# Performance work log

Measured on AMD Instinct MI355X. Metric: run time of the kernel, lower is better.

Reference implementation:

```python
import jax, jax.numpy as jnp
import numpy as np
import math

B, T, D_IN, D_OUT = 4, 2048, 2048, 2048

def _inv_sigmoid(v):
    return math.log(v / (1 - v + 1e-08))

def setup_inputs() -> dict:
    key = jax.random.key(0)
    ks = jax.random.split(key, 6)
    x = jax.random.normal(ks[0], (B, T, D_IN), dtype=jnp.float32)
    W_p = jax.random.normal(ks[1], (D_OUT, D_IN), dtype=jnp.float32) * 0.02
    W_i = jax.random.normal(ks[2], (D_OUT, D_IN), dtype=jnp.float32) * 0.002
    W_d = jax.random.normal(ks[3], (D_OUT, D_IN), dtype=jnp.float32) * 0.002
    alpha_logit = jnp.full((D_IN,), _inv_sigmoid(0.9), dtype=jnp.float32)
    beta_logit = jnp.full((D_IN,), _inv_sigmoid(0.5), dtype=jnp.float32)
    W_gate_w = jax.random.normal(ks[4], (3, 3 * D_IN), dtype=jnp.float32) * 0.01
    W_gate_b = jnp.array([1.0, 0.0, 0.0], dtype=jnp.float32)
    bias = jnp.zeros((D_OUT,), dtype=jnp.float32)
    return {"x": x, "W_p": W_p, "W_i": W_i, "W_d": W_d,
            "alpha_logit": alpha_logit, "beta_logit": beta_logit,
            "W_gate_w": W_gate_w, "W_gate_b": W_gate_b, "bias": bias}

def _pid_features(x, alpha, beta):
    # x: (B,T,D). Single scan computing EMA integral and smoothed derivative.
    x_t = jnp.swapaxes(x, 0, 1)  # (T,B,D)
    x_prev = jnp.concatenate([jnp.zeros_like(x_t[:1]), x_t[:-1]], axis=0)
    diff_t = x_t - x_prev  # raw finite difference
    def step(carry, inp):
        s, d = carry
        xt, dt = inp
        s = alpha * s + (1.0 - alpha) * xt
        d = beta * d + (1.0 - beta) * dt
        return (s, d), (s, d)
    s0 = jnp.zeros(x.shape[::2], dtype=x.dtype)  # (B,D)
    _, (integ_t, deriv_t) = jax.lax.scan(step, (s0, s0), (x_t, diff_t))
    return jnp.swapaxes(integ_t, 0, 1), jnp.swapaxes(deriv_t, 0, 1)

def reference(x, W_p, W_i, W_d, alpha_logit, beta_logit, W_gate_w, W_gate_b, bias):
    alpha = jax.nn.sigmoid(alpha_logit)  # (D,)
    beta = jax.nn.sigmoid(beta_logit)
    integral, derivative = _pid_features(x, alpha, beta)  # (B,T,D) each
    gate_in = jnp.concatenate([x, integral, derivative], axis=-1)  # (B,T,3D)
    logits = jnp.einsum('btk,gk->btg', gate_in, W_gate_w) + W_gate_b
    gates = jax.nn.softmax(logits, axis=-1)  # (B,T,3)
    p_out = jnp.einsum('btd,od->bto', x, W_p)
    i_out = jnp.einsum('btd,od->bto', integral, W_i)
    d_out = jnp.einsum('btd,od->bto', derivative, W_d)
    y = gates[..., 0:1] * p_out + gates[..., 1:2] * i_out + gates[..., 2:3] * d_out + bias
    return y
```

## Files before the change

### kernel.cpp

```cpp
#include <hip/hip_runtime.h>
#include <stdint.h>

typedef unsigned short u16;

#define GAS __attribute__((address_space(1)))
#define LAS __attribute__((address_space(3)))

typedef __bf16 bf16x8 __attribute__((ext_vector_type(8)));
typedef float f32x4 __attribute__((ext_vector_type(4)));


__device__ inline u16 f2b(float f) {
    uint32_t x = __float_as_uint(f);
    uint32_t r = (x + 0x7fffu + ((x >> 16) & 1u)) >> 16;
    return (u16)r;
}

__device__ inline float b2f(u16 u) {
    union { uint32_t i; float f; } v;
    v.i = ((uint32_t)u) << 16;
    return v.f;
}

__device__ inline void load8b(float* v, const u16* p) {
    uint4 u = *(const uint4*)p;
    v[0] = b2f((u16)(u.x)); v[1] = b2f((u16)(u.x >> 16));
    v[2] = b2f((u16)(u.y)); v[3] = b2f((u16)(u.y >> 16));
    v[4] = b2f((u16)(u.z)); v[5] = b2f((u16)(u.z >> 16));
    v[6] = b2f((u16)(u.w)); v[7] = b2f((u16)(u.w >> 16));
}

__device__ inline void load8f(float* v, const float* p) {
    float4 a = *(const float4*)p;
    float4 b = *(const float4*)(p + 4);
    v[0] = a.x; v[1] = a.y; v[2] = a.z; v[3] = a.w;
    v[4] = b.x; v[5] = b.y; v[6] = b.z; v[7] = b.w;
}

__device__ inline void store8b(u16* p, const float* v, float scale) {
    uint4 u;
    u.x = (uint32_t)f2b(v[0] * scale) | ((uint32_t)f2b(v[1] * scale) << 16);
    u.y = (uint32_t)f2b(v[2] * scale) | ((uint32_t)f2b(v[3] * scale) << 16);
    u.z = (uint32_t)f2b(v[4] * scale) | ((uint32_t)f2b(v[5] * scale) << 16);
    u.w = (uint32_t)f2b(v[6] * scale) | ((uint32_t)f2b(v[7] * scale) << 16);
    *(uint4*)p = u;
}

__device__ inline float sigmoidf(float v) { return 1.f / (1.f + __expf(-v)); }

__device__ inline float pow64f(float a) {
    float p = a * a;
    p = p * p;
    p = p * p;
    p = p * p;
    p = p * p;
    return p * p;
}

__device__ inline float* carry_ptr(u16* Z, int plane, int b, int c, int d) {
    int f = ((plane * 4 + b) * 32 + c) * 2048 + d;
    int row = f >> 10;
    int off = f & 1023;
    return (float*)(Z + (size_t)row * 6144) + off;
}

__global__ __launch_bounds__(256) void pack_w(
    const float* __restrict__ Wp, const float* __restrict__ Wi,
    const float* __restrict__ Wd, u16* __restrict__ Wcat)
{
    int i = (blockIdx.x * 256 + threadIdx.x) * 8;
    int seg = i >> 22;
    int j = i & 4194303;
    const float* src = (seg == 0) ? Wp : (seg == 1) ? Wi : Wd;
    int o = j >> 11;
    int c = j & 2047;
    float v[8];
    load8f(v, src + j);
    store8b(Wcat + (size_t)o * 6144 + seg * 2048 + c, v, 1.0f);
}

__global__ __launch_bounds__(256) void scan_pass1(
    const float* __restrict__ x, const float* __restrict__ alog,
    const float* __restrict__ blog, u16* __restrict__ Z)
{
    const int d = (blockIdx.x * 256 + threadIdx.x) * 2;
    const int c = blockIdx.y;
    const int b = blockIdx.z;
    const float2 al2 = *(const float2*)(alog + d);
    const float2 bl2 = *(const float2*)(blog + d);
    const float a0 = sigmoidf(al2.x), a1 = sigmoidf(al2.y);
    const float e0 = sigmoidf(bl2.x), e1 = sigmoidf(bl2.y);
    const float oa0 = 1.f - a0, oa1 = 1.f - a1;
    const float oe0 = 1.f - e0, oe1 = 1.f - e1;
    const float* xp = x + ((size_t)b * 2048 + c * 64) * 2048 + d;
    float px0 = 0.f, px1 = 0.f;
    if (c != 0) { float2 t = *(const float2*)(xp - 2048); px0 = t.x; px1 = t.y; }
    float s0 = 0.f, s1 = 0.f, d0 = 0.f, d1 = 0.f;
    #pragma unroll 8
    for (int t = 0; t < 64; ++t) {
        float2 xf = *(const float2*)(xp + (size_t)t * 2048);
        s0 = a0 * s0 + oa0 * xf.x;
        s1 = a1 * s1 + oa1 * xf.y;
        d0 = e0 * d0 + oe0 * (xf.x - px0);
        d1 = e1 * d1 + oe1 * (xf.y - px1);
        px0 = xf.x; px1 = xf.y;
    }
    *(float2*)carry_ptr(Z, 0, b, c, d) = make_float2(s0, s1);
    *(float2*)carry_ptr(Z, 1, b, c, d) = make_float2(d0, d1);
}

__global__ __launch_bounds__(256) void scan_pass2(
    const float* __restrict__ alog, const float* __restrict__ blog,
    u16* __restrict__ Z)
{
    const int g = blockIdx.x * 256 + threadIdx.x;
    const int b = g >> 11;
    const int d = g & 2047;
    const float aL = pow64f(sigmoidf(alog[d]));
    const float bL = pow64f(sigmoidf(blog[d]));
    float sIn = 0.f, dIn = 0.f;
    for (int c = 0; c < 32; ++c) {
        float* sp = carry_ptr(Z, 0, b, c, d);
        float* dp = carry_ptr(Z, 1, b, c, d);
        float sl = *sp, dl = *dp;
        *sp = sIn; *dp = dIn;
        sIn = sl + aL * sIn;
        dIn = dl + bL * dIn;
    }
}

__global__ __launch_bounds__(256) void scan_pass3(
    const float* __restrict__ x, const float* __restrict__ alog,
    const float* __restrict__ blog, u16* __restrict__ Z)
{
    const int d = (blockIdx.x * 256 + threadIdx.x) * 2;
    const int c = blockIdx.y;
    const int b = blockIdx.z;
    const float2 al2 = *(const float2*)(alog + d);
    const float2 bl2 = *(const float2*)(blog + d);
    const float a0 = sigmoidf(al2.x), a1 = sigmoidf(al2.y);
    const float e0 = sigmoidf(bl2.x), e1 = sigmoidf(bl2.y);
    const float oa0 = 1.f - a0, oa1 = 1.f - a1;
    const float oe0 = 1.f - e0, oe1 = 1.f - e1;
    const float* xp = x + ((size_t)b * 2048 + c * 64) * 2048 + d;
    u16* zp = Z + ((size_t)b * 2048 + c * 64) * 6144 + 2048 + d;
    float2 sc = *(const float2*)carry_ptr(Z, 0, b, c, d);
    float2 dc = *(const float2*)carry_ptr(Z, 1, b, c, d);
    float s0 = sc.x, s1 = sc.y, d0 = dc.x, d1 = dc.y;
    float px0 = 0.f, px1 = 0.f;
    if (c != 0) { float2 t = *(const float2*)(xp - 2048); px0 = t.x; px1 = t.y; }
    #pragma unroll 8
    for (int t = 0; t < 64; ++t) {
        float2 xf = *(const float2*)(xp + (size_t)t * 2048);
        s0 = a0 * s0 + oa0 * xf.x;
        s1 = a1 * s1 + oa1 * xf.y;
        d0 = e0 * d0 + oe0 * (xf.x - px0);
        d1 = e1 * d1 + oe1 * (xf.y - px1);
        px0 = xf.x; px1 = xf.y;
        size_t zo = (size_t)t * 6144;
        *(uint32_t*)(zp + zo) = (uint32_t)f2b(s0) | ((uint32_t)f2b(s1) << 16);
        *(uint32_t*)(zp + zo + 2048) = (uint32_t)f2b(d0) | ((uint32_t)f2b(d1) << 16);
    }
}

__global__ __launch_bounds__(256) void gates_kernel(
    const float* __restrict__ x, const float* __restrict__ Wg,
    const float* __restrict__ Wgb, u16* __restrict__ Z)
{
    const int row = blockIdx.x;
    const int tid = threadIdx.x;
    const int k = tid * 8;
    const float* xr = x + (size_t)row * 2048;
    u16* zr = Z + (size_t)row * 6144;

    float xv[8], sv[8], dv[8];
    load8f(xv, xr + k);
    load8b(sv, zr + 2048 + k);
    load8b(dv, zr + 4096 + k);

    float p[3];
    #pragma unroll
    for (int gg = 0; gg < 3; ++gg) {
        float wx[8], ws[8], wd[8];
        load8f(wx, Wg + gg * 6144 + k);
        load8f(ws, Wg + gg * 6144 + 2048 + k);
        load8f(wd, Wg + gg * 6144 + 4096 + k);
        float acc = 0.f;
        #pragma unroll
        for (int j = 0; j < 8; ++j)
            acc += xv[j] * wx[j] + sv[j] * ws[j] + dv[j] * wd[j];
        p[gg] = acc;
    }

    #pragma unroll
    for (int off = 32; off > 0; off >>= 1) {
        p[0] += __shfl_down(p[0], off);
        p[1] += __shfl_down(p[1], off);
        p[2] += __shfl_down(p[2], off);
    }

    __shared__ float red[4][3];
    __shared__ float gsh[3];
    int wv = tid >> 6, lane = tid & 63;
    if (lane == 0) { red[wv][0] = p[0]; red[wv][1] = p[1]; red[wv][2] = p[2]; }
    __syncthreads();
    if (tid == 0) {
        float l0 = red[0][0] + red[1][0] + red[2][0] + red[3][0] + Wgb[0];
        float l1 = red[0][1] + red[1][1] + red[2][1] + red[3][1] + Wgb[1];
        float l2 = red[0][2] + red[1][2] + red[2][2] + red[3][2] + Wgb[2];
        float m = fmaxf(l0, fmaxf(l1, l2));
        float e0 = __expf(l0 - m), e1 = __expf(l1 - m), e2 = __expf(l2 - m);
        float inv = 1.f / (e0 + e1 + e2);
        gsh[0] = e0 * inv; gsh[1] = e1 * inv; gsh[2] = e2 * inv;
    }
    __syncthreads();
    float g0 = gsh[0], g1 = gsh[1], g2 = gsh[2];
    store8b(zr + k, xv, g0);
    store8b(zr + 2048 + k, sv, g1);
    store8b(zr + 4096 + k, dv, g2);
}

__global__ __launch_bounds__(512, 2) void gemm_kernel(
    const u16* __restrict__ Z, const u16* __restrict__ Wcat,
    const float* __restrict__ bias, float* __restrict__ out)
{
    extern __shared__ u16 lds[];
    u16* const lA = lds;
    u16* const lB = lds + 32768;

    const int tid = threadIdx.x;
    const int bn = blockIdx.x * 256;
    const int bm = blockIdx.y * 256;

    const int sr  = tid >> 3;
    const int scq = (tid & 7) ^ (sr & 7);
    const u16* aglob = Z    + (size_t)(bm + sr) * 6144 + scq * 8;
    const u16* bglob = Wcat + (size_t)(bn + sr) * 6144 + scq * 8;

    const int lane = tid & 63;
    const int wv = tid >> 6;
    const int wm = wv & 1;
    const int wn = wv >> 1;
    const int fr = lane & 15;
    const int fq = lane >> 4;
    const int chlo = fq ^ (fr & 7);
    const int aoff = fr * 64 + chlo * 8;
    const int boff = ((wn & 1) * 64 + fr) * 64 + chlo * 8;
    const int aoffh = aoff ^ 32;
    const int boffh = boff ^ 32;

    f32x4 acc[8][4] = {};

#define GLOAD(gsrc, ldst)                                                     \
    __builtin_amdgcn_global_load_lds((const GAS uint32_t*)(gsrc),             \
                                     (LAS uint32_t*)(ldst), 16, 0, 0)

    GLOAD(bglob,                        lB + tid * 8);
    GLOAD(bglob + (size_t) 64 * 6144,   lB + 4096 + tid * 8);
    GLOAD(bglob + (size_t)128 * 6144,   lB + 8192 + tid * 8);
    GLOAD(bglob + (size_t)192 * 6144,   lB + 8192 + 4096 + tid * 8);
    GLOAD(aglob,                        lA + tid * 8);
    GLOAD(aglob + (size_t)128 * 6144,   lA + 8192 + tid * 8);
    GLOAD(aglob + (size_t) 64 * 6144,   lA + 4096 + tid * 8);
    GLOAD(aglob + (size_t)192 * 6144,   lA + 8192 + 4096 + tid * 8);
    asm volatile("s_waitcnt vmcnt(2)" ::: "memory");
    __builtin_amdgcn_s_barrier();

    for (int kt = 0; kt < 96; ++kt) {
        const int pb  = (kt & 1) * 2;
        const int nbb = pb ^ 2;
        const int t1  = (kt < 95) ? kt + 1 : 95;
        const size_t kc = (size_t)t1 * 64;
        const u16* aS = lA + (pb + wm) * 8192;
        const u16* bS = lB + (pb + (wn >> 1)) * 8192;
        bf16x8 av[4], bv[4];

        #pragma unroll
        for (int i = 0; i < 4; ++i) av[i] = *(const bf16x8*)(aS + aoff + i * 1024);
        #pragma unroll
        for (int j = 0; j < 4; ++j) bv[j] = *(const bf16x8*)(bS + boff + j * 1024);
        GLOAD(bglob + kc,                      lB + nbb * 8192 + tid * 8);
        GLOAD(bglob + (size_t)64 * 6144 + kc,  lB + nbb * 8192 + 4096 + tid * 8);
        __builtin_amdgcn_s_barrier();
        asm volatile("s_waitcnt lgkmcnt(0)" ::: "memory");
        __builtin_amdgcn_s_setprio(1);
        #pragma unroll
        for (int i = 0; i < 4; ++i)
            #pragma unroll
            for (int j = 0; j < 4; ++j)
                acc[i][j] = __builtin_amdgcn_mfma_f32_16x16x32_bf16(
                    av[i], bv[j], acc[i][j], 0, 0, 0);
        __builtin_amdgcn_s_setprio(0);
        asm volatile("s_waitcnt vmcnt(2)" ::: "memory");
        __builtin_amdgcn_s_barrier();

        #pragma unroll
        for (int i = 0; i < 4; ++i)
            av[i] = *(const bf16x8*)(aS + aoff + 4096 + i * 1024);
        GLOAD(bglob + (size_t)128 * 6144 + kc, lB + (nbb + 1) * 8192 + tid * 8);
        GLOAD(bglob + (size_t)192 * 6144 + kc, lB + (nbb + 1) * 8192 + 4096 + tid * 8);
        __builtin_amdgcn_s_barrier();
        asm volatile("s_waitcnt lgkmcnt(0)" ::: "memory");
        __builtin_amdgcn_s_setprio(1);
        #pragma unroll
        for (int i = 0; i < 4; ++i)
            #pragma unroll
            for (int j = 0; j < 4; ++j)
                acc[4 + i][j] = __builtin_amdgcn_mfma_f32_16x16x32_bf16(
                    av[i], bv[j], acc[4 + i][j], 0, 0, 0);
        __builtin_amdgcn_s_setprio(0);
        __builtin_amdgcn_s_barrier();

        #pragma unroll
        for (int i = 0; i < 4; ++i) av[i] = *(const bf16x8*)(aS + aoffh + i * 1024);
        #pragma unroll
        for (int j = 0; j < 4; ++j) bv[j] = *(const bf16x8*)(bS + boffh + j * 1024);
        GLOAD(aglob + kc,                      lA + nbb * 8192 + tid * 8);
        GLOAD(aglob + (size_t)128 * 6144 + kc, lA + (nbb + 1) * 8192 + tid * 8);
        __builtin_amdgcn_s_barrier();
        asm volatile("s_waitcnt lgkmcnt(0)" ::: "memory");
        __builtin_amdgcn_s_setprio(1);
        #pragma unroll
        for (int i = 0; i < 4; ++i)
            #pragma unroll
            for (int j = 0; j < 4; ++j)
                acc[i][j] = __builtin_amdgcn_mfma_f32_16x16x32_bf16(
                    av[i], bv[j], acc[i][j], 0, 0, 0);
        __builtin_amdgcn_s_setprio(0);
        __builtin_amdgcn_s_barrier();

        #pragma unroll
        for (int i = 0; i < 4; ++i)
            av[i] = *(const bf16x8*)(aS + aoffh + 4096 + i * 1024);
        GLOAD(aglob + (size_t) 64 * 6144 + kc, lA + nbb * 8192 + 4096 + tid * 8);
        GLOAD(aglob + (size_t)192 * 6144 + kc, lA + (nbb + 1) * 8192 + 4096 + tid * 8);
        __builtin_amdgcn_s_barrier();
        asm volatile("s_waitcnt lgkmcnt(0)" ::: "memory");
        __builtin_amdgcn_s_setprio(1);
        #pragma unroll
        for (int i = 0; i < 4; ++i)
            #pragma unroll
            for (int j = 0; j < 4; ++j)
                acc[4 + i][j] = __builtin_amdgcn_mfma_f32_16x16x32_bf16(
                    av[i], bv[j], acc[4 + i][j], 0, 0, 0);
        __builtin_amdgcn_s_setprio(0);
        asm volatile("s_waitcnt vmcnt(2)" ::: "memory");
        __builtin_amdgcn_s_barrier();
    }

    asm volatile("s_waitcnt vmcnt(0)" ::: "memory");

    #pragma unroll
    for (int j = 0; j < 4; ++j) {
        const int col = bn + wn * 64 + j * 16 + fr;
        const float bb = bias[col];
        #pragma unroll
        for (int mf = 0; mf < 8; ++mf) {
            const int row0 = bm + wm * 128 + mf * 16 + fq * 4;
            #pragma unroll
            for (int r = 0; r < 4; ++r)
                out[(size_t)(row0 + r) * 2048 + col] = acc[mf][j][r] + bb;
        }
    }
#undef GLOAD
}

extern "C" void kernel_launch(void* const* d_in, const int* in_sizes, int n_in,
                              void* d_out, int out_size, void* d_ws, size_t ws_size,
                              hipStream_t stream) {
    const float* x    = (const float*)d_in[0];
    const float* Wp   = (const float*)d_in[1];
    const float* Wi   = (const float*)d_in[2];
    const float* Wd   = (const float*)d_in[3];
    const float* al   = (const float*)d_in[4];
    const float* bl   = (const float*)d_in[5];
    const float* Wg   = (const float*)d_in[6];
    const float* Wgb  = (const float*)d_in[7];
    const float* bias = (const float*)d_in[8];
    float* out = (float*)d_out;

    u16* Z    = (u16*)d_ws;
    u16* Wcat = (u16*)((char*)d_ws + (size_t)8192 * 6144 * 2);

    static bool lds_cfgd = false;
    if (!lds_cfgd) {
        (void)hipFuncSetAttribute((const void*)gemm_kernel,
                                  hipFuncAttributeMaxDynamicSharedMemorySize,
                                  131072);
        lds_cfgd = true;
    }

    pack_w<<<6144, 256, 0, stream>>>(Wp, Wi, Wd, Wcat);
    scan_pass1<<<dim3(4, 32, 4), 256, 0, stream>>>(x, al, bl, Z);
    scan_pass2<<<32, 256, 0, stream>>>(al, bl, Z);
    scan_pass3<<<dim3(4, 32, 4), 256, 0, stream>>>(x, al, bl, Z);
    gates_kernel<<<8192, 256, 0, stream>>>(x, Wg, Wgb, Z);
    gemm_kernel<<<dim3(8, 32), 512, 131072, stream>>>(Z, Wcat, bias, out);
}
```

Before: 397.9 us.

## Shorten scan chunks for more parallelism and restructure gates kernel per-wave

The chunked scan now uses 128 chunks of 16 timesteps instead of 32 chunks of 64, which gives the scan passes 4x more blocks and shorter serial chains. The cost is a longer serial carry propagation in pass2. The gates kernel stages the gate weights in shared memory once per block and has each wave handle whole rows, reducing with shuffles only. This removes the per-row block syncs and the repeated global weight loads, at the price of 72KB of LDS per block, which limits occupancy.

```diff
diff --git a/kernel.cpp b/kernel.cpp
--- a/kernel.cpp
+++ b/kernel.cpp
@@ -48,17 +48,16 @@
 
 __device__ inline float sigmoidf(float v) { return 1.f / (1.f + __expf(-v)); }
 
-__device__ inline float pow64f(float a) {
+__device__ inline float pow16f(float a) {
     float p = a * a;
     p = p * p;
     p = p * p;
     p = p * p;
-    p = p * p;
-    return p * p;
+    return p;
 }
 
 __device__ inline float* carry_ptr(u16* Z, int plane, int b, int c, int d) {
-    int f = ((plane * 4 + b) * 32 + c) * 2048 + d;
+    int f = ((plane * 4 + b) * 128 + c) * 2048 + d;
     int row = f >> 10;
     int off = f & 1023;
     return (float*)(Z + (size_t)row * 6144) + off;
@@ -92,12 +91,12 @@
     const float e0 = sigmoidf(bl2.x), e1 = sigmoidf(bl2.y);
     const float oa0 = 1.f - a0, oa1 = 1.f - a1;
     const float oe0 = 1.f - e0, oe1 = 1.f - e1;
-    const float* xp = x + ((size_t)b * 2048 + c * 64) * 2048 + d;
+    const float* xp = x + ((size_t)b * 2048 + c * 16) * 2048 + d;
     float px0 = 0.f, px1 = 0.f;
     if (c != 0) { float2 t = *(const float2*)(xp - 2048); px0 = t.x; px1 = t.y; }
     float s0 = 0.f, s1 = 0.f, d0 = 0.f, d1 = 0.f;
-    #pragma unroll 8
-    for (int t = 0; t < 64; ++t) {
+    #pragma unroll
+    for (int t = 0; t < 16; ++t) {
         float2 xf = *(const float2*)(xp + (size_t)t * 2048);
         s0 = a0 * s0 + oa0 * xf.x;
         s1 = a1 * s1 + oa1 * xf.y;
@@ -116,10 +115,11 @@
     const int g = blockIdx.x * 256 + threadIdx.x;
     const int b = g >> 11;
     const int d = g & 2047;
-    const float aL = pow64f(sigmoidf(alog[d]));
-    const float bL = pow64f(sigmoidf(blog[d]));
+    const float aL = pow16f(sigmoidf(alog[d]));
+    const float bL = pow16f(sigmoidf(blog[d]));
     float sIn = 0.f, dIn = 0.f;
-    for (int c = 0; c < 32; ++c) {
+    #pragma unroll 4
+    for (int c = 0; c < 128; ++c) {
         float* sp = carry_ptr(Z, 0, b, c, d);
         float* dp = carry_ptr(Z, 1, b, c, d);
         float sl = *sp, dl = *dp;
@@ -142,15 +142,15 @@
     const float e0 = sigmoidf(bl2.x), e1 = sigmoidf(bl2.y);
     const float oa0 = 1.f - a0, oa1 = 1.f - a1;
     const float oe0 = 1.f - e0, oe1 = 1.f - e1;
-    const float* xp = x + ((size_t)b * 2048 + c * 64) * 2048 + d;
-    u16* zp = Z + ((size_t)b * 2048 + c * 64) * 6144 + 2048 + d;
+    const float* xp = x + ((size_t)b * 2048 + c * 16) * 2048 + d;
+    u16* zp = Z + ((size_t)b * 2048 + c * 16) * 6144 + 2048 + d;
     float2 sc = *(const float2*)carry_ptr(Z, 0, b, c, d);
     float2 dc = *(const float2*)carry_ptr(Z, 1, b, c, d);
     float s0 = sc.x, s1 = sc.y, d0 = dc.x, d1 = dc.y;
     float px0 = 0.f, px1 = 0.f;
     if (c != 0) { float2 t = *(const float2*)(xp - 2048); px0 = t.x; px1 = t.y; }
-    #pragma unroll 8
-    for (int t = 0; t < 64; ++t) {
+    #pragma unroll
+    for (int t = 0; t < 16; ++t) {
         float2 xf = *(const float2*)(xp + (size_t)t * 2048);
         s0 = a0 * s0 + oa0 * xf.x;
         s1 = a1 * s1 + oa1 * xf.y;
@@ -167,57 +167,74 @@
     const float* __restrict__ x, const float* __restrict__ Wg,
     const float* __restrict__ Wgb, u16* __restrict__ Z)
 {
-    const int row = blockIdx.x;
+    extern __shared__ float wsh[];
     const int tid = threadIdx.x;
-    const int k = tid * 8;
-    const float* xr = x + (size_t)row * 2048;
-    u16* zr = Z + (size_t)row * 6144;
-
-    float xv[8], sv[8], dv[8];
-    load8f(xv, xr + k);
-    load8b(sv, zr + 2048 + k);
-    load8b(dv, zr + 4096 + k);
-
-    float p[3];
+
     #pragma unroll
-    for (int gg = 0; gg < 3; ++gg) {
-        float wx[8], ws[8], wd[8];
-        load8f(wx, Wg + gg * 6144 + k);
-        load8f(ws, Wg + gg * 6144 + 2048 + k);
-        load8f(wd, Wg + gg * 6144 + 4096 + k);
-        float acc = 0.f;
-        #pragma unroll
-        for (int j = 0; j < 8; ++j)
-            acc += xv[j] * wx[j] + sv[j] * ws[j] + dv[j] * wd[j];
-        p[gg] = acc;
-    }
+    for (int i = tid; i < 4608; i += 256)
+        ((float4*)wsh)[i] = ((const float4*)Wg)[i];
+    __syncthreads();
+
+    const int wv = tid >> 6;
+    const int lane = tid & 63;
+    const float b0 = Wgb[0], b1 = Wgb[1], b2 = Wgb[2];
 
     #pragma unroll
-    for (int off = 32; off > 0; off >>= 1) {
-        p[0] += __shfl_down(p[0], off);
-        p[1] += __shfl_down(p[1], off);
-        p[2] += __shfl_down(p[2], off);
-    }
-
-    __shared__ float red[4][3];
-    __shared__ float gsh[3];
-    int wv = tid >> 6, lane = tid & 63;
-    if (lane == 0) { red[wv][0] = p[0]; red[wv][1] = p[1]; red[wv][2] = p[2]; }
-    __syncthreads();
-    if (tid == 0) {
-        float l0 = red[0][0] + red[1][0] + red[2][0] + red[3][0] + Wgb[0];
-        float l1 = red[0][1] + red[1][1] + red[2][1] + red[3][1] + Wgb[1];
-        float l2 = red[0][2] + red[1][2] + red[2][2] + red[3][2] + Wgb[2];
-        float m = fmaxf(l0, fmaxf(l1, l2));
-        float e0 = __expf(l0 - m), e1 = __expf(l1 - m), e2 = __expf(l2 - m);
-        float inv = 1.f / (e0 + e1 + e2);
-        gsh[0] = e0 * inv; gsh[1] = e1 * inv; gsh[2] = e2 * inv;
-    }
-    __syncthreads();
-    float g0 = gsh[0], g1 = gsh[1], g2 = gsh[2];
-    store8b(zr + k, xv, g0);
-    store8b(zr + 2048 + k, sv, g1);
-    store8b(zr + 4096 + k, dv, g2);
+    for (int r = 0; r < 4; ++r) {
+        const int row = blockIdx.x * 16 + wv * 4 + r;
+        const float* xr = x + (size_t)row * 2048;
+        u16* zr = Z + (size_t)row * 6144;
+
+        float xv[4][8], sv[4][8], dv[4][8];
+        #pragma unroll
+        for (int part = 0; part < 4; ++part) {
+            const int k = part * 512 + lane * 8;
+            load8f(xv[part], xr + k);
+            load8b(sv[part], zr + 2048 + k);
+            load8b(dv[part], zr + 4096 + k);
+        }
+
+        float p[3];
+        #pragma unroll
+        for (int gg = 0; gg < 3; ++gg) {
+            float acc = 0.f;
+            #pragma unroll
+            for (int part = 0; part < 4; ++part) {
+                const int k = part * 512 + lane * 8;
+                float wx[8], ws[8], wd[8];
+                load8f(wx, wsh + gg * 6144 + k);
+                load8f(ws, wsh + gg * 6144 + 2048 + k);
+                load8f(wd, wsh + gg * 6144 + 4096 + k);
+                #pragma unroll
+                for (int j = 0; j < 8; ++j)
+                    acc += xv[part][j] * wx[j] + sv[part][j] * ws[j]
+                         + dv[part][j] * wd[j];
+            }
+            p[gg] = acc;
+        }
+
+        #pragma unroll
+        for (int off = 32; off > 0; off >>= 1) {
+            p[0] += __shfl_down(p[0], off);
+            p[1] += __shfl_down(p[1], off);
+            p[2] += __shfl_down(p[2], off);
+        }
+        const float l0 = __shfl(p[0], 0) + b0;
+        const float l1 = __shfl(p[1], 0) + b1;
+        const float l2 = __shfl(p[2], 0) + b2;
+        const float m = fmaxf(l0, fmaxf(l1, l2));
+        const float e0 = __expf(l0 - m), e1 = __expf(l1 - m), e2 = __expf(l2 - m);
+        const float inv = 1.f / (e0 + e1 + e2);
+        const float g0 = e0 * inv, g1 = e1 * inv, g2 = e2 * inv;
+
+        #pragma unroll
+        for (int part = 0; part < 4; ++part) {
+            const int k = part * 512 + lane * 8;
+            store8b(zr + k, xv[part], g0);
+            store8b(zr + 2048 + k, sv[part], g1);
+            store8b(zr + 4096 + k, dv[part], g2);
+        }
+    }
 }
 
 __global__ __launch_bounds__(512, 2) void gemm_kernel(
@@ -387,13 +404,16 @@
         (void)hipFuncSetAttribute((const void*)gemm_kernel,
                                   hipFuncAttributeMaxDynamicSharedMemorySize,
                                   131072);
+        (void)hipFuncSetAttribute((const void*)gates_kernel,
+                                  hipFuncAttributeMaxDynamicSharedMemorySize,
+                                  73728);
         lds_cfgd = true;
     }
 
     pack_w<<<6144, 256, 0, stream>>>(Wp, Wi, Wd, Wcat);
-    scan_pass1<<<dim3(4, 32, 4), 256, 0, stream>>>(x, al, bl, Z);
+    scan_pass1<<<dim3(4, 128, 4), 256, 0, stream>>>(x, al, bl, Z);
     scan_pass2<<<32, 256, 0, stream>>>(al, bl, Z);
-    scan_pass3<<<dim3(4, 32, 4), 256, 0, stream>>>(x, al, bl, Z);
-    gates_kernel<<<8192, 256, 0, stream>>>(x, Wg, Wgb, Z);
+    scan_pass3<<<dim3(4, 128, 4), 256, 0, stream>>>(x, al, bl, Z);
+    gates_kernel<<<512, 256, 73728, stream>>>(x, Wg, Wgb, Z);
     gemm_kernel<<<dim3(8, 32), 512, 131072, stream>>>(Z, Wcat, bias, out);
 }
```

Measured after the change: 577.0 us. 45.0% more time.
